# Performance work log

Hardware: AMD Instinct MI355X
Metric: run time of the kernel (lower is better)

The kernel has to match this reference:

```python
import jax, jax.numpy as jnp
import numpy as np

B, S, D, H, G = 2, 4096, 768, 12, 64
HD = D // H
W = 256              # one-sided window (attention_window=512); also the chunk size
NC = S // W
NEG = -1e9
SCALE = 1.0 / np.sqrt(HD)


def setup_inputs() -> dict:
    key = jax.random.key(0)
    ks = jax.random.split(key, 9)
    lin = lambda k: 0.02 * jax.random.normal(k, (D, D), dtype=jnp.float32)
    zb = lambda: jnp.zeros((D,), jnp.float32)
    return {
        "query": jax.random.normal(ks[0], (S, B, D), dtype=jnp.float32),
        # 0 = local token, -1 = global token (wrapper multiplies by -1 -> +1 = global in HF convention)
        "key_padding_mask": jnp.zeros((B, S), jnp.int32).at[:, :G].set(-1),
        "Wq": lin(ks[1]), "bq": zb(),
        "Wk": lin(ks[2]), "bk": zb(),
        "Wv": lin(ks[3]), "bv": zb(),
        "Wqg": lin(ks[4]), "bqg": zb(),
        "Wkg": lin(ks[5]), "bkg": zb(),
        "Wvg": lin(ks[6]), "bvg": zb(),
        "Wo": lin(ks[7]), "bo": zb(),
    }


def _heads(x):  # [B,S,D] -> [B,H,S,HD]
    return x.reshape(B, S, H, HD).transpose(0, 2, 1, 3)


def reference(query, key_padding_mask, Wq, bq, Wk, bk, Wv, bv,
              Wqg, bqg, Wkg, bkg, Wvg, bvg, Wo, bo):
    x = query.transpose(1, 0, 2)                      # [B,S,D]
    attn_mask = -key_padding_mask                     # wrapper: key_padding_mask * -1
    is_pad = attn_mask < 0                            # [B,S]
    is_glb = attn_mask > 0

    q = _heads(x @ Wq + bq) * SCALE                   # [B,H,S,HD]
    k = _heads(x @ Wk + bk)
    v = _heads(x @ Wv + bv)

    # ---- sliding-window scores via overlapping 3-chunk key blocks ----
    qc = q.reshape(B, H, NC, W, HD)
    blk_idx = jnp.arange(NC)[:, None] * W + jnp.arange(3 * W)[None, :]   # [NC,3W] into padded seq
    kpad = jnp.pad(k, ((0, 0), (0, 0), (W, W), (0, 0)))
    vpad = jnp.pad(v, ((0, 0), (0, 0), (W, W), (0, 0)))
    kblk = kpad[:, :, blk_idx]                        # [B,H,NC,3W,HD]
    vblk = vpad[:, :, blk_idx]
    local = jnp.einsum('bhcqd,bhckd->bhcqk', qc, kblk)  # [B,H,NC,W,3W]

    rel = jnp.arange(3 * W)[None, :] - jnp.arange(W)[:, None] - W        # key pos - query pos
    jpos = (jnp.arange(NC)[:, None, None] - 1) * W + jnp.arange(3 * W)[None, None, :]
    band_ok = (jnp.abs(rel)[None] <= W) & (jpos >= 0) & (jpos < S)       # [NC,W,3W]

    key_bad = is_pad | is_glb                         # pad keys masked; global keys handled separately
    kb_blk = jnp.pad(key_bad, ((0, 0), (W, W)), constant_values=True)[:, blk_idx]  # [B,NC,3W]
    ok = band_ok[None, None] & ~kb_blk[:, None, :, None, :]
    local = jnp.where(ok, local, NEG)

    # ---- all queries -> global keys (first G tokens), regular K/V ----
    gsc = jnp.einsum('bhqd,bhgd->bhqg', q, k[:, :, :G])                  # [B,H,S,G]

    scores = jnp.concatenate([gsc, local.reshape(B, H, S, 3 * W)], axis=-1)
    probs = jax.nn.softmax(scores, axis=-1)
    pg = probs[..., :G]
    pl = probs[..., G:].reshape(B, H, NC, W, 3 * W)

    out = jnp.einsum('bhcqk,bhckd->bhcqd', pl, vblk).reshape(B, H, S, HD)
    out = out + jnp.einsum('bhqg,bhgd->bhqd', pg, v[:, :, :G])

    # ---- global query rows: full attention with the dedicated global projections ----
    qg = (_heads(x @ Wqg + bqg) * SCALE)[:, :, :G]    # [B,H,G,HD]
    kg = _heads(x @ Wkg + bkg)
    vg = _heads(x @ Wvg + bvg)
    gq = jnp.einsum('bhgd,bhkd->bhgk', qg, kg)        # [B,H,G,S]
    gq = jnp.where(is_pad[:, None, None, :], NEG, gq)
    gp = jax.nn.softmax(gq, axis=-1)
    out = out.at[:, :, :G].set(jnp.einsum('bhgk,bhkd->bhgd', gp, vg))

    attn_out = out.transpose(0, 2, 1, 3).reshape(B, S, D)   # merge heads -> [B,S,D]
    attn_out = attn_out.transpose(1, 0, 2)                  # back to [S,B,D]
    return attn_out @ Wo + bo                               # wrapper's output Linear
```

## Files before the change

### kernel.cpp

```cpp
#include <hip/hip_runtime.h>
#include <hip/hip_bf16.h>
#include <cstdint>

#define BB 2
#define SS 4096
#define DD 768
#define HH 12
#define GG 64
#define WW 256

typedef __hip_bfloat16 bf16;
typedef unsigned short u16;
typedef __attribute__((ext_vector_type(8))) short short8v;
typedef __attribute__((ext_vector_type(4))) float floatx4;

__device__ __forceinline__ float b2f(u16 u) {
  return __uint_as_float(((unsigned int)u) << 16);
}
__device__ __forceinline__ u16 f2bu(float f) {
  bf16 h = __float2bfloat16(f);
  return *reinterpret_cast<u16*>(&h);
}
__device__ __forceinline__ void async_copy16(const u16* g, u16* l) {
  __builtin_amdgcn_global_load_lds(
      (const __attribute__((address_space(1))) void*)g,
      (__attribute__((address_space(3))) void*)l, 16, 0, 0);
}

struct P7 { const void* p[7]; };

__global__ __launch_bounds__(256) void detect_dtype(const u16* __restrict__ q,
                                                    int* __restrict__ flag) {
  __shared__ int cnt;
  int tid = threadIdx.x;
  if (tid == 0) cnt = 0;
  __syncthreads();
  int bad = 0;
#pragma unroll
  for (int i = 0; i < 16; ++i) {
    float f = b2f(q[tid * 16 + i]);
    if (!isfinite(f) || fabsf(f) > 100.f) bad++;
  }
  atomicAdd(&cnt, bad);
  __syncthreads();
  if (tid == 0) *flag = (cnt > 256) ? 1 : 0;
}

__global__ __launch_bounds__(256) void canon_bf16(const void* __restrict__ src,
                                                  bf16* __restrict__ dst, int n,
                                                  const int* __restrict__ flag) {
  bool f32 = (*flag != 0);
  for (int i = blockIdx.x * 256 + threadIdx.x; i < n; i += gridDim.x * 256) {
    float v = f32 ? ((const float*)src)[i] : b2f(((const u16*)src)[i]);
    dst[i] = __float2bfloat16(v);
  }
}

__global__ __launch_bounds__(256) void transpose_w7(P7 srcs, bf16* __restrict__ dst,
                                                    const int* __restrict__ flag) {
  __shared__ float tile[32][33];
  bool f32 = (*flag != 0);
  const void* src = srcs.p[blockIdx.z];
  bf16* d = dst + (size_t)blockIdx.z * DD * DD;
  int tx = threadIdx.x & 31, ty = threadIdx.x >> 5;
  int k0 = blockIdx.x * 32, n0 = blockIdx.y * 32;
#pragma unroll
  for (int i = 0; i < 32; i += 8) {
    int k = k0 + ty + i, n = n0 + tx;
    float v = f32 ? ((const float*)src)[(size_t)k * DD + n]
                  : b2f(((const u16*)src)[(size_t)k * DD + n]);
    tile[ty + i][tx] = v;
  }
  __syncthreads();
#pragma unroll
  for (int i = 0; i < 32; i += 8) {
    int n = n0 + ty + i, k = k0 + tx;
    d[(size_t)n * DD + k] = __float2bfloat16(tile[tx][ty + i]);
  }
}

__global__ __launch_bounds__(256) void canon_bias7(P7 srcs, bf16* __restrict__ dst,
                                                   const int* __restrict__ flag) {
  bool f32 = (*flag != 0);
  int which = blockIdx.x;
  const void* s = srcs.p[which];
  for (int j = threadIdx.x; j < DD; j += 256)
    dst[which * DD + j] =
        __float2bfloat16(f32 ? ((const float*)s)[j] : b2f(((const u16*)s)[j]));
}

__device__ __forceinline__ void gemm_core(const u16* __restrict__ Xp,
                                          const u16* __restrict__ Wp, int bm,
                                          int bn, int tid, u16 (*As)[32],
                                          u16 (*Bs)[32], floatx4 (&acc)[4][4]) {
  int lane = tid & 63, w = tid >> 6, quad = lane >> 4, t = lane & 15;
  int wm = (w >> 1) * 64, wn = (w & 1) * 64;
  int lr = lane >> 2, lc = (lane & 3) * 8;
  for (int k0 = 0; k0 < DD; k0 += 32) {
    __syncthreads();
#pragma unroll
    for (int i = 0; i < 2; ++i) {
      async_copy16(Xp + (size_t)(bm + w * 32 + i * 16 + lr) * DD + k0 + lc,
                   &As[w * 32 + i * 16][0]);
      async_copy16(Wp + (size_t)(bn + w * 32 + i * 16 + lr) * DD + k0 + lc,
                   &Bs[w * 32 + i * 16][0]);
    }
    __syncthreads();
    short8v a[4], bb[4];
#pragma unroll
    for (int mt = 0; mt < 4; ++mt)
      a[mt] = *(const short8v*)&As[wm + mt * 16 + t][quad * 8];
#pragma unroll
    for (int nt = 0; nt < 4; ++nt)
      bb[nt] = *(const short8v*)&Bs[wn + nt * 16 + t][quad * 8];
#pragma unroll
    for (int mt = 0; mt < 4; ++mt)
#pragma unroll
      for (int nt = 0; nt < 4; ++nt)
        acc[mt][nt] = __builtin_amdgcn_mfma_f32_16x16x32_bf16(
            a[mt], bb[nt], acc[mt][nt], 0, 0, 0);
  }
}

__global__ __launch_bounds__(256) void gemm5(const bf16* __restrict__ Xb,
                                             const bf16* __restrict__ Wt0,
                                             const bf16* __restrict__ b0,
                                             bf16* __restrict__ out0) {
  __shared__ __align__(16) u16 As[128][32];
  __shared__ __align__(16) u16 Bs[128][32];
  int tid = threadIdx.x, lane = tid & 63, w = tid >> 6, quad = lane >> 4,
      t = lane & 15;
  int wm = (w >> 1) * 64, wn = (w & 1) * 64;
  int by = blockIdx.y, which = by / 6, bn = (by % 6) * 128,
      bm = blockIdx.x * 128;
  const u16* Wp = (const u16*)Wt0 + (size_t)which * DD * DD;
  const u16* bias = (const u16*)b0 + which * DD;
  bf16* outp = out0 + (size_t)which * BB * HH * SS * 64;
  float scale = (which == 0) ? 0.125f : 1.f;
  bool tr = (which == 2) || (which == 4);
  floatx4 acc[4][4];
#pragma unroll
  for (int i = 0; i < 4; ++i)
#pragma unroll
    for (int j = 0; j < 4; ++j) acc[i][j] = (floatx4)(0.f);
  gemm_core((const u16*)Xb, Wp, bm, bn, tid, As, Bs, acc);
#pragma unroll
  for (int nt = 0; nt < 4; ++nt) {
    int n = bn + wn + nt * 16 + t;
    int h = n >> 6, hd = n & 63;
    float bi = b2f(bias[n]);
#pragma unroll
    for (int mt = 0; mt < 4; ++mt) {
#pragma unroll
      for (int r = 0; r < 4; ++r) {
        int m = bm + wm + mt * 16 + quad * 4 + r;
        int s = m >> 1, b = m & 1;
        float val = (acc[mt][nt][r] + bi) * scale;
        size_t addr = tr ? ((size_t)((b * HH + h) * 64 + hd)) * SS + s
                         : (((size_t)(b * HH + h)) * SS + s) * 64 + hd;
        outp[addr] = __float2bfloat16(val);
      }
    }
  }
}

template <int MODE>
__global__ __launch_bounds__(256) void gemm_one(const bf16* __restrict__ Xb,
                                                const bf16* __restrict__ Wtb,
                                                const bf16* __restrict__ biasb,
                                                void* __restrict__ outv,
                                                int Sdim, float scale) {
  __shared__ __align__(16) u16 As[128][32];
  __shared__ __align__(16) u16 Bs[128][32];
  int tid = threadIdx.x, lane = tid & 63, w = tid >> 6, quad = lane >> 4,
      t = lane & 15;
  int wm = (w >> 1) * 64, wn = (w & 1) * 64;
  int bm = blockIdx.x * 128, bn = blockIdx.y * 128;
  floatx4 acc[4][4];
#pragma unroll
  for (int i = 0; i < 4; ++i)
#pragma unroll
    for (int j = 0; j < 4; ++j) acc[i][j] = (floatx4)(0.f);
  gemm_core((const u16*)Xb, (const u16*)Wtb, bm, bn, tid, As, Bs, acc);
  const u16* bias = (const u16*)biasb;
#pragma unroll
  for (int nt = 0; nt < 4; ++nt) {
    int n = bn + wn + nt * 16 + t;
    float bi = b2f(bias[n]);
#pragma unroll
    for (int mt = 0; mt < 4; ++mt) {
#pragma unroll
      for (int r = 0; r < 4; ++r) {
        int m = bm + wm + mt * 16 + quad * 4 + r;
        float val = (acc[mt][nt][r] + bi) * scale;
        if (MODE == 0) {
          int s = m >> 1, b = m & 1;
          int h = n >> 6, hd = n & 63;
          ((bf16*)outv)[(((size_t)(b * HH + h)) * Sdim + s) * 64 + hd] =
              __float2bfloat16(val);
        } else {
          ((float*)outv)[(size_t)m * DD + n] = val;
        }
      }
    }
  }
}

template <int GLB>
__global__ __launch_bounds__(256) void attn_mfma(
    const bf16* __restrict__ qb, const bf16* __restrict__ kb,
    const bf16* __restrict__ vtb, const int* __restrict__ kpm,
    bf16* __restrict__ attnout, float* __restrict__ part) {
  __shared__ __align__(16) u16 Qs[64][72];
  __shared__ __align__(16) u16 Ks[64][72];
  __shared__ __align__(16) u16 Vt[64][72];
  __shared__ __align__(16) u16 Ps[64][72];
  __shared__ int kbadS[64];
  int bid = blockIdx.x;
  int bh, sblk = 0, seg = 0;
  if (!GLB) {
    sblk = bid & 63;
    if (sblk == 0) return;
    bh = bid >> 6;
  } else {
    bh = bid >> 4;
    seg = bid & 15;
  }
  int b = bh / HH, h = bh % HH;
  int tid = threadIdx.x, lane = tid & 63, w = tid >> 6;
  int quad = lane >> 4, t = lane & 15;
  const u16* qp = GLB ? (const u16*)qb + (size_t)bh * GG * 64
                      : (const u16*)qb + (size_t)bh * SS * 64;
  const u16* kp = (const u16*)kb + (size_t)bh * SS * 64;
  const u16* vp = (const u16*)vtb + (size_t)bh * SS * 64;
  int sq0 = GLB ? 0 : sblk * 64;
  int srow = tid >> 2, scol = (tid & 3) * 16;
#pragma unroll
  for (int i = 0; i < 4; ++i)
    *(ushort4*)&Qs[srow][scol + 4 * i] =
        *(const ushort4*)(qp + (size_t)(sq0 + srow) * 64 + scol + 4 * i);
  __syncthreads();
  short8v aq[2];
#pragma unroll
  for (int ks = 0; ks < 2; ++ks)
    aq[ks] = *(const short8v*)&Qs[16 * w + t][ks * 32 + quad * 8];
  floatx4 O[4];
#pragma unroll
  for (int i = 0; i < 4; ++i) O[i] = (floatx4)(0.f);
  float ps[4] = {0.f, 0.f, 0.f, 0.f};
  int iters, kb_lo = 0;
  if (GLB) {
    iters = 4;
  } else {
    int win_lo = max(sq0 - WW, GG);
    int win_hi = min(sq0 + 63 + WW, SS - 1);
    kb_lo = win_lo & ~63;
    iters = ((win_hi - kb_lo) >> 6) + 2;
  }
  for (int it = 0; it < iters; ++it) {
    int kbs = GLB ? (seg << 8) + (it << 6)
                  : ((it == 0) ? 0 : kb_lo + ((it - 1) << 6));
    ushort4 ku[4], vu[4];
#pragma unroll
    for (int i = 0; i < 4; ++i) {
      ku[i] = *(const ushort4*)(kp + (size_t)(kbs + srow) * 64 + scol + 4 * i);
      vu[i] = *(const ushort4*)(vp + (size_t)srow * SS + kbs + scol + 4 * i);
    }
    int kbval = (tid < 64) ? kpm[b * SS + kbs + tid] : 0;
    __syncthreads();
#pragma unroll
    for (int i = 0; i < 4; ++i) {
      *(ushort4*)&Ks[srow][scol + 4 * i] = ku[i];
      *(ushort4*)&Vt[srow][scol + 4 * i] = vu[i];
    }
    if (tid < 64) kbadS[tid] = kbval;
    __syncthreads();
    floatx4 S[4];
#pragma unroll
    for (int nt = 0; nt < 4; ++nt) {
      S[nt] = (floatx4)(0.f);
#pragma unroll
      for (int ks = 0; ks < 2; ++ks) {
        short8v bk = *(const short8v*)&Ks[nt * 16 + t][ks * 32 + quad * 8];
        S[nt] = __builtin_amdgcn_mfma_f32_16x16x32_bf16(aq[ks], bk, S[nt], 0, 0, 0);
      }
    }
    if (GLB) {
#pragma unroll
      for (int nt = 0; nt < 4; ++nt) {
        int bad = kbadS[nt * 16 + t];
#pragma unroll
        for (int r = 0; r < 4; ++r) {
          float p = __expf((bad <= 0) ? S[nt][r] : -3.0e38f);
          ps[r] += p;
          Ps[16 * w + quad * 4 + r][((nt ^ quad) << 4) + t] = f2bu(p);
        }
      }
    } else if (it == 0) {
#pragma unroll
      for (int nt = 0; nt < 4; ++nt)
#pragma unroll
        for (int r = 0; r < 4; ++r) {
          float p = __expf(S[nt][r]);
          ps[r] += p;
          Ps[16 * w + quad * 4 + r][((nt ^ quad) << 4) + t] = f2bu(p);
        }
    } else {
#pragma unroll
      for (int r = 0; r < 4; ++r) {
        int qr = sq0 + 16 * w + quad * 4 + r;
        int off = kbs + t + WW - qr;
#pragma unroll
        for (int nt = 0; nt < 4; ++nt) {
          int bad = kbadS[nt * 16 + t];
          unsigned u = (unsigned)(off + nt * 16);
          float p = __expf((u <= 2 * WW && bad == 0) ? S[nt][r] : -3.0e38f);
          ps[r] += p;
          Ps[16 * w + quad * 4 + r][((nt ^ quad) << 4) + t] = f2bu(p);
        }
      }
    }
    short8v ap[2];
#pragma unroll
    for (int ks = 0; ks < 2; ++ks) {
      int chunk = (2 * ks + (quad >> 1)) ^ ((t >> 2) & 3);
      ap[ks] = *(const short8v*)&Ps[16 * w + t][(chunk << 4) + ((quad & 1) << 3)];
    }
#pragma unroll
    for (int dt = 0; dt < 4; ++dt)
#pragma unroll
      for (int ks = 0; ks < 2; ++ks) {
        short8v bv = *(const short8v*)&Vt[dt * 16 + t][ks * 32 + quad * 8];
        O[dt] = __builtin_amdgcn_mfma_f32_16x16x32_bf16(ap[ks], bv, O[dt], 0, 0, 0);
      }
  }
#pragma unroll
  for (int r = 0; r < 4; ++r)
#pragma unroll
    for (int off = 1; off < 16; off <<= 1) ps[r] += __shfl_xor(ps[r], off);
  if (!GLB) {
#pragma unroll
    for (int dt = 0; dt < 4; ++dt)
#pragma unroll
      for (int r = 0; r < 4; ++r) {
        int qr = sq0 + 16 * w + quad * 4 + r;
        attnout[((size_t)qr * BB + b) * DD + h * 64 + dt * 16 + t] =
            __float2bfloat16(O[dt][r] / ps[r]);
      }
  } else {
    float* pO = part + (size_t)bid * 4160;
#pragma unroll
    for (int dt = 0; dt < 4; ++dt)
#pragma unroll
      for (int r = 0; r < 4; ++r)
        pO[(16 * w + quad * 4 + r) * 64 + dt * 16 + t] = O[dt][r];
    if (t == 0)
#pragma unroll
      for (int r = 0; r < 4; ++r) pO[4096 + 16 * w + quad * 4 + r] = ps[r];
  }
}

__global__ __launch_bounds__(256) void attn_comb(const float* __restrict__ part,
                                                 bf16* __restrict__ attnout) {
  int tid = threadIdx.x, lane = tid & 63, w = tid >> 6;
  int idx = blockIdx.x * 4 + w;
  int bh = idx >> 6, row = idx & 63;
  int b = bh / HH, h = bh % HH;
  float o = 0.f, L = 0.f;
#pragma unroll
  for (int s16 = 0; s16 < 16; ++s16) {
    const float* p = part + (size_t)(bh * 16 + s16) * 4160;
    o += p[(row << 6) + lane];
    L += p[4096 + row];
  }
  attnout[((size_t)row * BB + b) * DD + h * 64 + lane] = __float2bfloat16(o / L);
}

extern "C" void kernel_launch(void* const* d_in, const int* in_sizes, int n_in,
                              void* d_out, int out_size, void* d_ws,
                              size_t ws_size, hipStream_t stream) {
  const int* kpm = (const int*)d_in[1];
  float* outp = (float*)d_out;
  const size_t SZ = (size_t)BB * HH * SS * 64;
  const size_t WSZ = (size_t)DD * DD;
  bf16* p = (bf16*)d_ws;
  bf16* cQ = p; p += SZ;
  bf16* cWt = p; p += 7 * WSZ;
  bf16* cB = p; p += 7 * DD;
  bf16* q = p; p += SZ;
  bf16* k = p; p += SZ;
  bf16* v = p; p += SZ;
  bf16* kg = p; p += SZ;
  bf16* vg = p; p += SZ;
  bf16* qg = p; p += (size_t)BB * HH * GG * 64;
  bf16* attnout = p; p += SZ;
  float* part = (float*)p;
  int* flag = (int*)(part + (size_t)384 * 4160);
  const float SC = 0.125f;
  dim3 blk(256);

  P7 wsrc{{d_in[2], d_in[4], d_in[6], d_in[10], d_in[12], d_in[8], d_in[14]}};
  P7 bsrc{{d_in[3], d_in[5], d_in[7], d_in[11], d_in[13], d_in[9], d_in[15]}};

  detect_dtype<<<1, blk, 0, stream>>>((const u16*)d_in[0], flag);
  canon_bf16<<<dim3(2048), blk, 0, stream>>>(d_in[0], cQ, (int)SZ, flag);
  transpose_w7<<<dim3(24, 24, 7), blk, 0, stream>>>(wsrc, cWt, flag);
  canon_bias7<<<dim3(7), blk, 0, stream>>>(bsrc, cB, flag);

  gemm5<<<dim3(64, 30), blk, 0, stream>>>(cQ, cWt, cB, q);
  gemm_one<0><<<dim3(1, 6), blk, 0, stream>>>(cQ, cWt + 5 * WSZ, cB + 5 * DD,
                                              qg, GG, SC);
  attn_mfma<0><<<dim3(BB * HH * 64), blk, 0, stream>>>(q, k, v, kpm, attnout,
                                                       nullptr);
  attn_mfma<1><<<dim3(BB * HH * 16), blk, 0, stream>>>(qg, kg, vg, kpm, nullptr,
                                                       part);
  attn_comb<<<dim3(BB * HH * 16), blk, 0, stream>>>(part, attnout);
  gemm_one<1><<<dim3(64, 6), blk, 0, stream>>>(attnout, cWt + 6 * WSZ,
                                               cB + 6 * DD, outp, 0, 1.f);
}
```

Baseline: 313.1 us.

## Vectorize GEMM epilogues, transpose V separately, and use 128-row local attention tiles

The GEMM MFMA operands are swapped so each lane holds four consecutive output columns, which lets the epilogues write ushort4/float4 instead of scattered scalar stores. The transposed V layout is no longer written from the GEMM epilogue; dedicated tr_vt kernels transpose V and Vg afterwards, reusing freed buffers. Local attention moves to a 128-query tile kernel that uses async global-to-LDS copies, so each loaded K/V tile serves more queries. The changes add two extra transpose launches and a wider-tile kernel whose register pressure is capped by launch bounds of 3.

```diff
diff --git a/kernel.cpp b/kernel.cpp
--- a/kernel.cpp
+++ b/kernel.cpp
@@ -87,6 +87,33 @@
   for (int j = threadIdx.x; j < DD; j += 256)
     dst[which * DD + j] =
         __float2bfloat16(f32 ? ((const float*)s)[j] : b2f(((const u16*)s)[j]));
+}
+
+__global__ __launch_bounds__(256) void tr_vt(const bf16* __restrict__ src,
+                                             bf16* __restrict__ dst) {
+  __shared__ u16 T[64][66];
+  int stile = blockIdx.x, bh = blockIdx.y;
+  const u16* in = (const u16*)src + (size_t)bh * SS * 64;
+  u16* out = (u16*)dst + (size_t)bh * SS * 64;
+  int tid = threadIdx.x;
+  int srow = tid >> 2, scol = (tid & 3) * 16;
+#pragma unroll
+  for (int i = 0; i < 4; ++i) {
+    ushort4 u = *(const ushort4*)(in + (size_t)(stile * 64 + srow) * 64 + scol + 4 * i);
+    *(ushort2*)&T[srow][scol + 4 * i] = make_ushort2(u.x, u.y);
+    *(ushort2*)&T[srow][scol + 4 * i + 2] = make_ushort2(u.z, u.w);
+  }
+  __syncthreads();
+  int drow = tid >> 2, dcol = (tid & 3) * 16;
+#pragma unroll
+  for (int i = 0; i < 4; ++i) {
+    ushort4 u;
+    u.x = T[dcol + 4 * i + 0][drow];
+    u.y = T[dcol + 4 * i + 1][drow];
+    u.z = T[dcol + 4 * i + 2][drow];
+    u.w = T[dcol + 4 * i + 3][drow];
+    *(ushort4*)(out + (size_t)drow * SS + stile * 64 + dcol + 4 * i) = u;
+  }
 }
 
 __device__ __forceinline__ void gemm_core(const u16* __restrict__ Xp,
@@ -114,18 +141,18 @@
     for (int nt = 0; nt < 4; ++nt)
       bb[nt] = *(const short8v*)&Bs[wn + nt * 16 + t][quad * 8];
 #pragma unroll
-    for (int mt = 0; mt < 4; ++mt)
-#pragma unroll
-      for (int nt = 0; nt < 4; ++nt)
-        acc[mt][nt] = __builtin_amdgcn_mfma_f32_16x16x32_bf16(
-            a[mt], bb[nt], acc[mt][nt], 0, 0, 0);
-  }
-}
-
-__global__ __launch_bounds__(256) void gemm5(const bf16* __restrict__ Xb,
-                                             const bf16* __restrict__ Wt0,
-                                             const bf16* __restrict__ b0,
-                                             bf16* __restrict__ out0) {
+    for (int nt = 0; nt < 4; ++nt)
+#pragma unroll
+      for (int mt = 0; mt < 4; ++mt)
+        acc[nt][mt] = __builtin_amdgcn_mfma_f32_16x16x32_bf16(
+            bb[nt], a[mt], acc[nt][mt], 0, 0, 0);
+  }
+}
+
+__global__ __launch_bounds__(256, 3) void gemm5(const bf16* __restrict__ Xb,
+                                                const bf16* __restrict__ Wt0,
+                                                const bf16* __restrict__ b0,
+                                                bf16* __restrict__ out0) {
   __shared__ __align__(16) u16 As[128][32];
   __shared__ __align__(16) u16 Bs[128][32];
   int tid = threadIdx.x, lane = tid & 63, w = tid >> 6, quad = lane >> 4,
@@ -137,7 +164,6 @@
   const u16* bias = (const u16*)b0 + which * DD;
   bf16* outp = out0 + (size_t)which * BB * HH * SS * 64;
   float scale = (which == 0) ? 0.125f : 1.f;
-  bool tr = (which == 2) || (which == 4);
   floatx4 acc[4][4];
 #pragma unroll
   for (int i = 0; i < 4; ++i)
@@ -146,30 +172,30 @@
   gemm_core((const u16*)Xb, Wp, bm, bn, tid, As, Bs, acc);
 #pragma unroll
   for (int nt = 0; nt < 4; ++nt) {
-    int n = bn + wn + nt * 16 + t;
-    int h = n >> 6, hd = n & 63;
-    float bi = b2f(bias[n]);
+    int n0 = bn + wn + nt * 16 + quad * 4;
+    int h = n0 >> 6, hd0 = n0 & 63;
+    ushort4 bi4 = *(const ushort4*)&bias[n0];
+    float bia[4] = {b2f(bi4.x), b2f(bi4.y), b2f(bi4.z), b2f(bi4.w)};
 #pragma unroll
     for (int mt = 0; mt < 4; ++mt) {
-#pragma unroll
-      for (int r = 0; r < 4; ++r) {
-        int m = bm + wm + mt * 16 + quad * 4 + r;
-        int s = m >> 1, b = m & 1;
-        float val = (acc[mt][nt][r] + bi) * scale;
-        size_t addr = tr ? ((size_t)((b * HH + h) * 64 + hd)) * SS + s
-                         : (((size_t)(b * HH + h)) * SS + s) * 64 + hd;
-        outp[addr] = __float2bfloat16(val);
-      }
+      int m = bm + wm + mt * 16 + t;
+      int s = m >> 1, b = m & 1;
+      ushort4 o;
+      o.x = f2bu((acc[nt][mt][0] + bia[0]) * scale);
+      o.y = f2bu((acc[nt][mt][1] + bia[1]) * scale);
+      o.z = f2bu((acc[nt][mt][2] + bia[2]) * scale);
+      o.w = f2bu((acc[nt][mt][3] + bia[3]) * scale);
+      *(ushort4*)((u16*)outp + (((size_t)(b * HH + h)) * SS + s) * 64 + hd0) = o;
     }
   }
 }
 
 template <int MODE>
-__global__ __launch_bounds__(256) void gemm_one(const bf16* __restrict__ Xb,
-                                                const bf16* __restrict__ Wtb,
-                                                const bf16* __restrict__ biasb,
-                                                void* __restrict__ outv,
-                                                int Sdim, float scale) {
+__global__ __launch_bounds__(256, 3) void gemm_one(const bf16* __restrict__ Xb,
+                                                   const bf16* __restrict__ Wtb,
+                                                   const bf16* __restrict__ biasb,
+                                                   void* __restrict__ outv,
+                                                   int Sdim, float scale) {
   __shared__ __align__(16) u16 As[128][32];
   __shared__ __align__(16) u16 Bs[128][32];
   int tid = threadIdx.x, lane = tid & 63, w = tid >> 6, quad = lane >> 4,
@@ -185,60 +211,200 @@
   const u16* bias = (const u16*)biasb;
 #pragma unroll
   for (int nt = 0; nt < 4; ++nt) {
-    int n = bn + wn + nt * 16 + t;
-    float bi = b2f(bias[n]);
+    int n0 = bn + wn + nt * 16 + quad * 4;
+    ushort4 bi4 = *(const ushort4*)&bias[n0];
+    float bia[4] = {b2f(bi4.x), b2f(bi4.y), b2f(bi4.z), b2f(bi4.w)};
 #pragma unroll
     for (int mt = 0; mt < 4; ++mt) {
-#pragma unroll
-      for (int r = 0; r < 4; ++r) {
-        int m = bm + wm + mt * 16 + quad * 4 + r;
-        float val = (acc[mt][nt][r] + bi) * scale;
-        if (MODE == 0) {
-          int s = m >> 1, b = m & 1;
-          int h = n >> 6, hd = n & 63;
-          ((bf16*)outv)[(((size_t)(b * HH + h)) * Sdim + s) * 64 + hd] =
-              __float2bfloat16(val);
-        } else {
-          ((float*)outv)[(size_t)m * DD + n] = val;
-        }
-      }
-    }
-  }
-}
-
-template <int GLB>
-__global__ __launch_bounds__(256) void attn_mfma(
+      int m = bm + wm + mt * 16 + t;
+      if (MODE == 0) {
+        int s = m >> 1, b = m & 1;
+        int h = n0 >> 6, hd0 = n0 & 63;
+        ushort4 o;
+        o.x = f2bu((acc[nt][mt][0] + bia[0]) * scale);
+        o.y = f2bu((acc[nt][mt][1] + bia[1]) * scale);
+        o.z = f2bu((acc[nt][mt][2] + bia[2]) * scale);
+        o.w = f2bu((acc[nt][mt][3] + bia[3]) * scale);
+        *(ushort4*)((u16*)outv + (((size_t)(b * HH + h)) * Sdim + s) * 64 + hd0) = o;
+      } else {
+        float4 o;
+        o.x = (acc[nt][mt][0] + bia[0]) * scale;
+        o.y = (acc[nt][mt][1] + bia[1]) * scale;
+        o.z = (acc[nt][mt][2] + bia[2]) * scale;
+        o.w = (acc[nt][mt][3] + bia[3]) * scale;
+        *(float4*)((float*)outv + (size_t)m * DD + n0) = o;
+      }
+    }
+  }
+}
+
+__global__ __launch_bounds__(256, 3) void attn_local128(
     const bf16* __restrict__ qb, const bf16* __restrict__ kb,
     const bf16* __restrict__ vtb, const int* __restrict__ kpm,
-    bf16* __restrict__ attnout, float* __restrict__ part) {
+    bf16* __restrict__ attnout) {
+  __shared__ __align__(16) u16 Qs[128][64];
+  __shared__ __align__(16) u16 Ks[64][64];
+  __shared__ __align__(16) u16 Vt[64][64];
+  __shared__ __align__(16) u16 Ps[128][72];
+  __shared__ float Ls[128];
+  __shared__ int kbadS[64];
+  int bid = blockIdx.x;
+  int tile = bid & 31, bh = bid >> 5;
+  int b = bh / HH, h = bh % HH;
+  int tid = threadIdx.x, lane = tid & 63, w = tid >> 6;
+  int quad = lane >> 4, t = lane & 15;
+  const u16* qp = (const u16*)qb + (size_t)bh * SS * 64;
+  const u16* kp = (const u16*)kb + (size_t)bh * SS * 64;
+  const u16* vp = (const u16*)vtb + (size_t)bh * SS * 64;
+  int sq0 = GG + tile * 128;
+#pragma unroll
+  for (int j = 0; j < 4; ++j) {
+    int qr = sq0 + w * 32 + j * 8 + (lane >> 3);
+    int sr = qr < SS ? qr : SS - 1;
+    async_copy16(qp + (size_t)sr * 64 + (lane & 7) * 8, &Qs[w * 32 + j * 8][0]);
+  }
+  __syncthreads();
+  short8v aq[2][2];
+#pragma unroll
+  for (int st = 0; st < 2; ++st)
+#pragma unroll
+    for (int ks = 0; ks < 2; ++ks)
+      aq[st][ks] = *(const short8v*)&Qs[w * 32 + st * 16 + t][ks * 32 + quad * 8];
+  floatx4 O[2][4];
+#pragma unroll
+  for (int st = 0; st < 2; ++st)
+#pragma unroll
+    for (int dt = 0; dt < 4; ++dt) O[st][dt] = (floatx4)(0.f);
+  float ps[2][4] = {};
+  int win_lo = max(sq0 - WW, GG);
+  int win_hi = min(sq0 + 127 + WW, SS - 1);
+  int kb_lo = win_lo & ~63;
+  int iters = ((win_hi - kb_lo) >> 6) + 2;
+  for (int it = 0; it < iters; ++it) {
+    int kbs = (it == 0) ? 0 : kb_lo + ((it - 1) << 6);
+    __syncthreads();
+#pragma unroll
+    for (int j = 0; j < 2; ++j) {
+      async_copy16(kp + (size_t)(kbs + w * 16 + j * 8 + (lane >> 3)) * 64 +
+                       (lane & 7) * 8,
+                   &Ks[w * 16 + j * 8][0]);
+      async_copy16(vp + (size_t)(w * 16 + j * 8 + (lane >> 3)) * SS + kbs +
+                       (lane & 7) * 8,
+                   &Vt[w * 16 + j * 8][0]);
+    }
+    if (tid < 64) kbadS[tid] = kpm[b * SS + kbs + tid];
+    __syncthreads();
+#pragma unroll
+    for (int st = 0; st < 2; ++st) {
+      floatx4 S[4];
+#pragma unroll
+      for (int nt = 0; nt < 4; ++nt) {
+        S[nt] = (floatx4)(0.f);
+#pragma unroll
+        for (int ks = 0; ks < 2; ++ks) {
+          short8v bk = *(const short8v*)&Ks[nt * 16 + t][ks * 32 + quad * 8];
+          S[nt] = __builtin_amdgcn_mfma_f32_16x16x32_bf16(aq[st][ks], bk, S[nt],
+                                                          0, 0, 0);
+        }
+      }
+      int prow = w * 32 + st * 16 + quad * 4;
+      if (it == 0) {
+#pragma unroll
+        for (int nt = 0; nt < 4; ++nt)
+#pragma unroll
+          for (int r = 0; r < 4; ++r) {
+            float p = __expf(S[nt][r]);
+            ps[st][r] += p;
+            Ps[prow + r][((nt ^ quad) << 4) + t] = f2bu(p);
+          }
+      } else {
+#pragma unroll
+        for (int r = 0; r < 4; ++r) {
+          int qr = sq0 + prow + r;
+          int off = kbs + t + WW - qr;
+#pragma unroll
+          for (int nt = 0; nt < 4; ++nt) {
+            int bad = kbadS[nt * 16 + t];
+            unsigned u = (unsigned)(off + nt * 16);
+            float p = __expf((u <= 2 * WW && bad == 0) ? S[nt][r] : -3.0e38f);
+            ps[st][r] += p;
+            Ps[prow + r][((nt ^ quad) << 4) + t] = f2bu(p);
+          }
+        }
+      }
+    }
+    short8v ap[2][2];
+#pragma unroll
+    for (int st = 0; st < 2; ++st)
+#pragma unroll
+      for (int ks = 0; ks < 2; ++ks) {
+        int chunk = (2 * ks + (quad >> 1)) ^ ((t >> 2) & 3);
+        ap[st][ks] = *(const short8v*)&Ps[w * 32 + st * 16 + t]
+                                        [(chunk << 4) + ((quad & 1) << 3)];
+      }
+#pragma unroll
+    for (int dt = 0; dt < 4; ++dt) {
+#pragma unroll
+      for (int ks = 0; ks < 2; ++ks) {
+        short8v av = *(const short8v*)&Vt[dt * 16 + t][ks * 32 + quad * 8];
+#pragma unroll
+        for (int st = 0; st < 2; ++st)
+          O[st][dt] = __builtin_amdgcn_mfma_f32_16x16x32_bf16(av, ap[st][ks],
+                                                              O[st][dt], 0, 0, 0);
+      }
+    }
+  }
+#pragma unroll
+  for (int st = 0; st < 2; ++st) {
+#pragma unroll
+    for (int r = 0; r < 4; ++r)
+#pragma unroll
+      for (int off = 1; off < 16; off <<= 1) ps[st][r] += __shfl_xor(ps[st][r], off);
+    if (t == 0)
+#pragma unroll
+      for (int r = 0; r < 4; ++r) Ls[w * 32 + st * 16 + quad * 4 + r] = ps[st][r];
+  }
+#pragma unroll
+  for (int st = 0; st < 2; ++st) {
+    int q = sq0 + w * 32 + st * 16 + t;
+    if (q < SS) {
+      float linv = 1.0f / Ls[w * 32 + st * 16 + t];
+#pragma unroll
+      for (int dt = 0; dt < 4; ++dt) {
+        ushort4 o;
+        o.x = f2bu(O[st][dt][0] * linv);
+        o.y = f2bu(O[st][dt][1] * linv);
+        o.z = f2bu(O[st][dt][2] * linv);
+        o.w = f2bu(O[st][dt][3] * linv);
+        *(ushort4*)((u16*)attnout + ((size_t)q * BB + b) * DD + h * 64 +
+                    dt * 16 + quad * 4) = o;
+      }
+    }
+  }
+}
+
+__global__ __launch_bounds__(256) void attn_glb(
+    const bf16* __restrict__ qgb, const bf16* __restrict__ kgb,
+    const bf16* __restrict__ vtb, const int* __restrict__ kpm,
+    float* __restrict__ part) {
   __shared__ __align__(16) u16 Qs[64][72];
   __shared__ __align__(16) u16 Ks[64][72];
   __shared__ __align__(16) u16 Vt[64][72];
   __shared__ __align__(16) u16 Ps[64][72];
   __shared__ int kbadS[64];
   int bid = blockIdx.x;
-  int bh, sblk = 0, seg = 0;
-  if (!GLB) {
-    sblk = bid & 63;
-    if (sblk == 0) return;
-    bh = bid >> 6;
-  } else {
-    bh = bid >> 4;
-    seg = bid & 15;
-  }
-  int b = bh / HH, h = bh % HH;
+  int bh = bid >> 4, seg = bid & 15;
+  int b = bh / HH;
   int tid = threadIdx.x, lane = tid & 63, w = tid >> 6;
   int quad = lane >> 4, t = lane & 15;
-  const u16* qp = GLB ? (const u16*)qb + (size_t)bh * GG * 64
-                      : (const u16*)qb + (size_t)bh * SS * 64;
-  const u16* kp = (const u16*)kb + (size_t)bh * SS * 64;
+  const u16* qp = (const u16*)qgb + (size_t)bh * GG * 64;
+  const u16* kp = (const u16*)kgb + (size_t)bh * SS * 64;
   const u16* vp = (const u16*)vtb + (size_t)bh * SS * 64;
-  int sq0 = GLB ? 0 : sblk * 64;
   int srow = tid >> 2, scol = (tid & 3) * 16;
 #pragma unroll
   for (int i = 0; i < 4; ++i)
     *(ushort4*)&Qs[srow][scol + 4 * i] =
-        *(const ushort4*)(qp + (size_t)(sq0 + srow) * 64 + scol + 4 * i);
+        *(const ushort4*)(qp + (size_t)srow * 64 + scol + 4 * i);
   __syncthreads();
   short8v aq[2];
 #pragma unroll
@@ -248,18 +414,8 @@
 #pragma unroll
   for (int i = 0; i < 4; ++i) O[i] = (floatx4)(0.f);
   float ps[4] = {0.f, 0.f, 0.f, 0.f};
-  int iters, kb_lo = 0;
-  if (GLB) {
-    iters = 4;
-  } else {
-    int win_lo = max(sq0 - WW, GG);
-    int win_hi = min(sq0 + 63 + WW, SS - 1);
-    kb_lo = win_lo & ~63;
-    iters = ((win_hi - kb_lo) >> 6) + 2;
-  }
-  for (int it = 0; it < iters; ++it) {
-    int kbs = GLB ? (seg << 8) + (it << 6)
-                  : ((it == 0) ? 0 : kb_lo + ((it - 1) << 6));
+  for (int it = 0; it < 4; ++it) {
+    int kbs = (seg << 8) + (it << 6);
     ushort4 ku[4], vu[4];
 #pragma unroll
     for (int i = 0; i < 4; ++i) {
@@ -285,39 +441,14 @@
         S[nt] = __builtin_amdgcn_mfma_f32_16x16x32_bf16(aq[ks], bk, S[nt], 0, 0, 0);
       }
     }
-    if (GLB) {
-#pragma unroll
-      for (int nt = 0; nt < 4; ++nt) {
-        int bad = kbadS[nt * 16 + t];
-#pragma unroll
-        for (int r = 0; r < 4; ++r) {
-          float p = __expf((bad <= 0) ? S[nt][r] : -3.0e38f);
-          ps[r] += p;
-          Ps[16 * w + quad * 4 + r][((nt ^ quad) << 4) + t] = f2bu(p);
-        }
-      }
-    } else if (it == 0) {
-#pragma unroll
-      for (int nt = 0; nt < 4; ++nt)
-#pragma unroll
-        for (int r = 0; r < 4; ++r) {
-          float p = __expf(S[nt][r]);
-          ps[r] += p;
-          Ps[16 * w + quad * 4 + r][((nt ^ quad) << 4) + t] = f2bu(p);
-        }
-    } else {
+#pragma unroll
+    for (int nt = 0; nt < 4; ++nt) {
+      int bad = kbadS[nt * 16 + t];
 #pragma unroll
       for (int r = 0; r < 4; ++r) {
-        int qr = sq0 + 16 * w + quad * 4 + r;
-        int off = kbs + t + WW - qr;
-#pragma unroll
-        for (int nt = 0; nt < 4; ++nt) {
-          int bad = kbadS[nt * 16 + t];
-          unsigned u = (unsigned)(off + nt * 16);
-          float p = __expf((u <= 2 * WW && bad == 0) ? S[nt][r] : -3.0e38f);
-          ps[r] += p;
-          Ps[16 * w + quad * 4 + r][((nt ^ quad) << 4) + t] = f2bu(p);
-        }
+        float p = __expf((bad <= 0) ? S[nt][r] : -3.0e38f);
+        ps[r] += p;
+        Ps[16 * w + quad * 4 + r][((nt ^ quad) << 4) + t] = f2bu(p);
       }
     }
     short8v ap[2];
@@ -338,26 +469,15 @@
   for (int r = 0; r < 4; ++r)
 #pragma unroll
     for (int off = 1; off < 16; off <<= 1) ps[r] += __shfl_xor(ps[r], off);
-  if (!GLB) {
-#pragma unroll
-    for (int dt = 0; dt < 4; ++dt)
-#pragma unroll
-      for (int r = 0; r < 4; ++r) {
-        int qr = sq0 + 16 * w + quad * 4 + r;
-        attnout[((size_t)qr * BB + b) * DD + h * 64 + dt * 16 + t] =
-            __float2bfloat16(O[dt][r] / ps[r]);
-      }
-  } else {
-    float* pO = part + (size_t)bid * 4160;
-#pragma unroll
-    for (int dt = 0; dt < 4; ++dt)
-#pragma unroll
-      for (int r = 0; r < 4; ++r)
-        pO[(16 * w + quad * 4 + r) * 64 + dt * 16 + t] = O[dt][r];
-    if (t == 0)
-#pragma unroll
-      for (int r = 0; r < 4; ++r) pO[4096 + 16 * w + quad * 4 + r] = ps[r];
-  }
+  float* pO = part + (size_t)bid * 4160;
+#pragma unroll
+  for (int dt = 0; dt < 4; ++dt)
+#pragma unroll
+    for (int r = 0; r < 4; ++r)
+      pO[(16 * w + quad * 4 + r) * 64 + dt * 16 + t] = O[dt][r];
+  if (t == 0)
+#pragma unroll
+    for (int r = 0; r < 4; ++r) pO[4096 + 16 * w + quad * 4 + r] = ps[r];
 }
 
 __global__ __launch_bounds__(256) void attn_comb(const float* __restrict__ part,
@@ -396,6 +516,8 @@
   bf16* attnout = p; p += SZ;
   float* part = (float*)p;
   int* flag = (int*)(part + (size_t)384 * 4160);
+  bf16* vT = cQ;
+  bf16* vgT = v;
   const float SC = 0.125f;
   dim3 blk(256);
 
@@ -410,10 +532,10 @@
   gemm5<<<dim3(64, 30), blk, 0, stream>>>(cQ, cWt, cB, q);
   gemm_one<0><<<dim3(1, 6), blk, 0, stream>>>(cQ, cWt + 5 * WSZ, cB + 5 * DD,
                                               qg, GG, SC);
-  attn_mfma<0><<<dim3(BB * HH * 64), blk, 0, stream>>>(q, k, v, kpm, attnout,
-                                                       nullptr);
-  attn_mfma<1><<<dim3(BB * HH * 16), blk, 0, stream>>>(qg, kg, vg, kpm, nullptr,
-                                                       part);
+  tr_vt<<<dim3(64, 24), blk, 0, stream>>>(v, vT);
+  tr_vt<<<dim3(64, 24), blk, 0, stream>>>(vg, vgT);
+  attn_local128<<<dim3(24 * 32), blk, 0, stream>>>(q, k, vT, kpm, attnout);
+  attn_glb<<<dim3(BB * HH * 16), blk, 0, stream>>>(qg, kg, vgT, kpm, part);
   attn_comb<<<dim3(BB * HH * 16), blk, 0, stream>>>(part, attnout);
   gemm_one<1><<<dim3(64, 6), blk, 0, stream>>>(attnout, cWt + 6 * WSZ,
                                                cB + 6 * DD, outp, 0, 1.f);
```

Result: faster. 304.4 us (-2.8%).
